# Kernel optimization log

Measured on AMD Instinct MI355X. Metric: run time of the kernel, lower is better.

The kernel has to match this reference:

```python
import jax, jax.numpy as jnp
import numpy as np
from jax import lax

LOG2PI = float(np.log(2.0 * np.pi))
N_K, N_T, N_C, N_D, N_SPK = 256, 128, 32, 10, 1000000

def _std_normal_logpdf(x):
    return -0.5 * (x * x + LOG2PI)

def _normal_logpdf(x, mu, log_sig):
    z = (x - mu) * jnp.exp(-log_sig)
    return -0.5 * (z * z + LOG2PI) - log_sig

def safe_log(x, minval=1e-10):
    return jnp.log(x + minval)

def setup_inputs() -> dict:
    key = jax.random.key(0)
    ks_ = jax.random.split(key, 8)
    s = jax.random.normal(ks_[0], (N_SPK, N_D), dtype=jnp.float32)
    y = jax.random.normal(ks_[1], (N_K, N_T), dtype=jnp.float32)
    ks = jax.random.randint(ks_[2], (N_SPK,), 0, N_K, dtype=jnp.int32)
    ts = jax.random.randint(ks_[3], (N_SPK,), 0, N_T, dtype=jnp.int32)
    means = jax.random.normal(ks_[4], (N_C, N_D), dtype=jnp.float32)
    A = jax.random.normal(ks_[5], (N_C, N_D, N_D), dtype=jnp.float32)
    covs = jnp.einsum('cij,ckj->cik', A, A) / N_D + jnp.eye(N_D, dtype=jnp.float32)
    b_mu = jax.random.normal(ks_[6], (N_C,), dtype=jnp.float32)
    b_log_sig = jax.random.normal(ks_[7], (N_C,), dtype=jnp.float32)
    beta_mu = jax.random.normal(jax.random.fold_in(key, 10), (N_C, N_T), dtype=jnp.float32)
    beta_log_sig = jax.random.normal(jax.random.fold_in(key, 11), (N_C, N_T), dtype=jnp.float32)
    return {"s": s, "y": y, "ks": ks, "ts": ts, "means": means, "covs": covs,
            "b_mu": b_mu, "b_log_sig": b_log_sig, "beta_mu": beta_mu, "beta_log_sig": beta_log_sig}

def _mvn_ll(s, means, covs):
    # ll[n, c] = MVN(means[c], covs[c]).log_prob(s[n]); loop over small n_c via lax.map
    L = jnp.linalg.cholesky(covs)                       # (c, d, d)
    logdet = 2.0 * jnp.sum(jnp.log(jnp.diagonal(L, axis1=1, axis2=2)), axis=1)  # (c,)
    d = s.shape[1]
    def comp(args):
        mu, Lc, ld = args
        diff = s - mu                                   # (n, d)
        z = jax.scipy.linalg.solve_triangular(Lc, diff.T, lower=True)  # (d, n)
        return -0.5 * (d * LOG2PI + ld + jnp.sum(z * z, axis=0))       # (n,)
    return lax.map(comp, (means, L, logdet)).T          # (n, c)

def reference(s, y, ks, ts, means, covs, b_mu, b_log_sig, beta_mu, beta_log_sig):
    # sampling=False path: use variational means
    b_sample, beta_sample = b_mu, beta_mu               # (c,), (c, t)
    # log_lambdas[k, c, t] = b[c] + beta[c, t] * y[k, t]
    log_lambdas = b_sample[None, :, None] + beta_sample[None, :, :] * y[:, None, :]
    log_pis = jax.nn.log_softmax(log_lambdas, axis=1)   # (k, c, t)
    ll = _mvn_ll(s, means, covs)                        # (n, c)
    logits = ll + log_pis[ks, :, ts]                    # per-spike gather -> (n, c)
    r = jax.nn.softmax(logits, axis=1)                  # responsibilities (n, c)
    log_prior = jnp.sum(_std_normal_logpdf(b_sample)) + jnp.sum(_std_normal_logpdf(beta_sample))
    log_q = jnp.sum(_normal_logpdf(b_sample, b_mu, b_log_sig)) + \
            jnp.sum(_normal_logpdf(beta_sample, beta_mu, beta_log_sig))
    elbo = log_prior - log_q
    elbo += jnp.sum(r * logits)
    elbo -= jnp.sum(r * safe_log(r))
    return elbo
```

## Files before the change

### kernel.cpp

```cpp
#include <hip/hip_runtime.h>
#include <hip/hip_bf16.h>
#include <math.h>

#define NK 256
#define NT 128
#define NC 32
#define ND 10
#define NSPK 1000000
#define LOG2PI 1.8378770664093453f
#define NCHUNK ((NSPK + 255) / 256)
#define GRID 1024

#define FSTR 36
#define LDS_DW (256 * FSTR)

typedef __attribute__((ext_vector_type(8))) short short8;
typedef __attribute__((ext_vector_type(4))) float floatx4;
typedef __attribute__((ext_vector_type(2))) float floatx2;
typedef __attribute__((ext_vector_type(4))) int intx4;

union FragCvt { intx4 i; short8 s; };


__device__ inline unsigned pack_bf16(float a, float b) {
  __hip_bfloat16 ha = __float2bfloat16(a), hb = __float2bfloat16(b);
  unsigned short ua, ub;
  __builtin_memcpy(&ua, &ha, 2);
  __builtin_memcpy(&ub, &hb, 2);
  return (unsigned)ua | ((unsigned)ub << 16);
}

__global__ __attribute__((amdgpu_waves_per_eu(1, 4)))
void prep_kernel(const float* __restrict__ y,
                 const float* __restrict__ means,
                 const float* __restrict__ covs,
                 const float* __restrict__ b_mu,
                 const float* __restrict__ b_ls,
                 const float* __restrict__ beta_mu,
                 const float* __restrict__ beta_ls,
                 int* __restrict__ wt,
                 float* __restrict__ cpack,
                 float* __restrict__ pisT,
                 double* __restrict__ acc,
                 unsigned int* __restrict__ counter) {
  int blk = blockIdx.x;
  int tid = threadIdx.x;

  if (blk == 0) {
    int c = tid;
    if (c >= NC) return;

    float M[ND][ND];
    #pragma unroll
    for (int i = 0; i < ND; ++i)
      #pragma unroll
      for (int j = 0; j < ND; ++j)
        M[i][j] = covs[c * ND * ND + i * ND + j];

    float logdet = 0.f;
    #pragma unroll
    for (int j = 0; j < ND; ++j) {
      float d = M[j][j];
      #pragma unroll
      for (int k = 0; k < ND; ++k) if (k < j) d -= M[j][k] * M[j][k];
      float sq = sqrtf(d);
      M[j][j] = sq;
      logdet += 2.f * __logf(sq);
      float inv = 1.f / sq;
      #pragma unroll
      for (int i = 0; i < ND; ++i) {
        if (i > j) {
          float s2 = M[i][j];
          #pragma unroll
          for (int k = 0; k < ND; ++k) if (k < j) s2 -= M[i][k] * M[j][k];
          M[i][j] = s2 * inv;
        }
      }
    }

    #pragma unroll
    for (int j = 0; j < ND; ++j) {
      M[j][j] = 1.f / M[j][j];
      #pragma unroll
      for (int i = 0; i < ND; ++i) {
        if (i > j) {
          float s2 = 0.f;
          #pragma unroll
          for (int k = 0; k < ND; ++k) if (k >= j && k < i) s2 += M[i][k] * M[k][j];
          M[i][j] = -s2 / M[i][i];
        }
      }
    }

    float pd[ND];
    #pragma unroll
    for (int i = 0; i < ND; ++i) {
      #pragma unroll
      for (int jj = 0; jj < ND; ++jj) {
        if (jj >= i) {
          float s2 = 0.f;
          #pragma unroll
          for (int k = 0; k < ND; ++k) if (k >= jj) s2 += M[k][i] * M[k][jj];
          if (jj > i) M[i][jj] = s2;
          else pd[i] = s2;
        }
      }
    }

    float mu[ND], q[ND];
    #pragma unroll
    for (int i = 0; i < ND; ++i) mu[i] = means[c * ND + i];
    float muPmu = 0.f;
    #pragma unroll
    for (int i = 0; i < ND; ++i) {
      float a2 = pd[i] * mu[i];
      #pragma unroll
      for (int j = 0; j < ND; ++j) {
        if (j < i) a2 += M[j][i] * mu[j];
        if (j > i) a2 += M[i][j] * mu[j];
      }
      q[i] = a2;
      muPmu += mu[i] * a2;
    }
    float cst = -0.5f * ((float)ND * LOG2PI + logdet + muPmu);

    float wv[64];
    int p = 0;
    #pragma unroll
    for (int i = 0; i < ND; ++i)
      #pragma unroll
      for (int j = 0; j < ND; ++j)
        if (j >= i && !(i == 9 && j == 9))
          wv[p++] = (i == j) ? -0.5f * pd[i] : -M[i][j];
    #pragma unroll
    for (int i = 0; i < ND; ++i) wv[54 + i] = q[i];

    #pragma unroll
    for (int j = 0; j < 32; ++j) {
      float a = wv[2 * j], b = wv[2 * j + 1];
      float ah = __bfloat162float(__float2bfloat16(a));
      float bh = __bfloat162float(__float2bfloat16(b));
      wt[c * 32 + j] = (int)pack_bf16(ah, bh);
      wt[(32 + c) * 32 + j] = (int)pack_bf16(a - ah, b - bh);
    }
    cpack[c] = cst;
    cpack[32 + c] = -0.5f * pd[9];

  } else if (blk == 1) {
    float local = 0.f;
    for (int i = tid; i < NC; i += 256)
      local += fmaf(-0.5f * b_mu[i], b_mu[i], b_ls[i]);
    for (int i = tid; i < NC * NT; i += 256)
      local += fmaf(-0.5f * beta_mu[i], beta_mu[i], beta_ls[i]);
    #pragma unroll
    for (int off = 32; off > 0; off >>= 1) local += __shfl_down(local, off);
    __shared__ float red[4];
    if ((tid & 63) == 0) red[tid >> 6] = local;
    __syncthreads();
    if (tid == 0) {
      acc[0] = (double)(red[0] + red[1] + red[2] + red[3]);
      counter[0] = 0u;
    }

  } else {
    int id = (blk - 2) * 256 + tid;
    int t = id & (NT - 1);
    float yv = y[id];
    float v[NC];
    float m = -1e30f;
    #pragma unroll
    for (int c = 0; c < NC; ++c) {
      v[c] = fmaf(beta_mu[c * NT + t], yv, b_mu[c]);
      m = fmaxf(m, v[c]);
    }
    float ssum = 0.f;
    #pragma unroll
    for (int c = 0; c < NC; ++c) ssum += __expf(v[c] - m);
    float lz = m + __logf(ssum);
    float* outp = pisT + (size_t)id * NC;
    #pragma unroll
    for (int c = 0; c < NC; ++c) outp[c] = v[c] - lz;
  }
}

__global__ __launch_bounds__(256) __attribute__((amdgpu_waves_per_eu(4, 4)))
void spike_kernel(const float* __restrict__ s,
                  const int* __restrict__ ks,
                  const int* __restrict__ ts,
                  const int* __restrict__ wt,
                  const float* __restrict__ cpack,
                  const float* __restrict__ pisT,
                  double* __restrict__ acc,
                  unsigned int* __restrict__ counter,
                  float* __restrict__ out) {
  __shared__ int lds[LDS_DW];
  __shared__ float red[4];

  int tid = threadIdx.x;
  int wv_ = tid >> 6, L = tid & 63;
  int r = L & 15, q = L >> 4;

  static constexpr int TI[64] = {
    0,0,0,0,0,0,0,0,0,0,
    1,1,1,1,1,1,1,1,1,
    2,2,2,2,2,2,2,2,
    3,3,3,3,3,3,3,
    4,4,4,4,4,4,
    5,5,5,5,5,
    6,6,6,6,
    7,7,7,
    8,8,
    0,1,2,3,4,5,6,7,8,9};
  static constexpr int TJ[64] = {
    0,1,2,3,4,5,6,7,8,9,
    1,2,3,4,5,6,7,8,9,
    2,3,4,5,6,7,8,9,
    3,4,5,6,7,8,9,
    4,5,6,7,8,9,
    5,6,7,8,9,
    6,7,8,9,
    7,8,9,
    8,9,
    -1,-1,-1,-1,-1,-1,-1,-1,-1,-1};

  FragCvt bf[2][2][2];
  #pragma unroll
  for (int h = 0; h < 2; ++h)
    #pragma unroll
    for (int nt = 0; nt < 2; ++nt)
      #pragma unroll
      for (int k2 = 0; k2 < 2; ++k2)
        bf[h][nt][k2].i =
            *(const intx4*)&wt[(h * 32 + nt * 16 + r) * 32 + k2 * 16 + q * 4];

  float lse_sum = 0.f;

  int ci = blockIdx.x;
  floatx4 sA, sB; floatx2 sC; int kk, tt;
  {
    int n = ci * 256 + tid;
    int nc = n < NSPK ? n : (NSPK - 1);
    const float* srow = s + (size_t)nc * ND;
    sA = __builtin_nontemporal_load((const floatx4*)srow);
    sB = __builtin_nontemporal_load((const floatx4*)(srow + 4));
    sC = __builtin_nontemporal_load((const floatx2*)(srow + 8));
    kk = __builtin_nontemporal_load(ks + nc);
    tt = __builtin_nontemporal_load(ts + nc);
  }

  for (; ci < NCHUNK; ci += GRID) {
    int n = ci * 256 + tid;
    float sv[10] = {sA.x, sA.y, sA.z, sA.w, sB.x, sB.y, sB.z, sB.w, sC.x, sC.y};
    float s9sq = sv[9] * sv[9];

    const float4* lpp = (const float4*)(pisT + (size_t)(kk * NT + tt) * NC);
    float4 lpv[8];
    #pragma unroll
    for (int i = 0; i < 8; ++i) lpv[i] = lpp[i];

    int cn = ci + GRID;
    if (cn < NCHUNK) {
      int n2 = cn * 256 + tid;
      int nc2 = n2 < NSPK ? n2 : (NSPK - 1);
      const float* srow2 = s + (size_t)nc2 * ND;
      sA = __builtin_nontemporal_load((const floatx4*)srow2);
      sB = __builtin_nontemporal_load((const floatx4*)(srow2 + 4));
      sC = __builtin_nontemporal_load((const floatx2*)(srow2 + 8));
      kk = __builtin_nontemporal_load(ks + nc2);
      tt = __builtin_nontemporal_load(ts + nc2);
    }

    {
      int rb = tid * FSTR;
      #pragma unroll
      for (int ch = 0; ch < 8; ++ch) {
        float t_[8];
        #pragma unroll
        for (int e = 0; e < 8; ++e) {
          int p = 8 * ch + e;
          t_[e] = (TJ[p] < 0) ? sv[TI[p]] : sv[TI[p]] * sv[TJ[p]];
        }
        intx4 v;
        v.x = (int)pack_bf16(t_[0], t_[1]);
        v.y = (int)pack_bf16(t_[2], t_[3]);
        v.z = (int)pack_bf16(t_[4], t_[5]);
        v.w = (int)pack_bf16(t_[6], t_[7]);
        *(intx4*)&lds[rb + ch * 4] = v;
      }
    }

    floatx4 accf[4][2];
    #pragma unroll
    for (int mt = 0; mt < 4; ++mt)
      #pragma unroll
      for (int nt = 0; nt < 2; ++nt)
        accf[mt][nt] = (floatx4){0.f, 0.f, 0.f, 0.f};

    #pragma unroll
    for (int mt = 0; mt < 4; ++mt) {
      #pragma unroll
      for (int k2 = 0; k2 < 2; ++k2) {
        FragCvt a;
        a.i = *(const intx4*)&lds[(wv_ * 64 + mt * 16 + r) * FSTR + k2 * 16 + q * 4];
        #pragma unroll
        for (int nt = 0; nt < 2; ++nt) {
          accf[mt][nt] = __builtin_amdgcn_mfma_f32_16x16x32_bf16(
              a.s, bf[0][nt][k2].s, accf[mt][nt], 0, 0, 0);
          accf[mt][nt] = __builtin_amdgcn_mfma_f32_16x16x32_bf16(
              a.s, bf[1][nt][k2].s, accf[mt][nt], 0, 0, 0);
        }
      }
    }

    #pragma unroll
    for (int mt = 0; mt < 4; ++mt)
      #pragma unroll
      for (int nt = 0; nt < 2; ++nt)
        #pragma unroll
        for (int rr = 0; rr < 4; ++rr) {
          int srow_ = wv_ * 64 + mt * 16 + q * 4 + rr;
          lds[srow_ * FSTR + nt * 16 + r] = __float_as_int(accf[mt][nt][rr]);
        }

    {
      float lp[32];
      #pragma unroll
      for (int i = 0; i < 8; ++i) {
        lp[4 * i + 0] = lpv[i].x; lp[4 * i + 1] = lpv[i].y;
        lp[4 * i + 2] = lpv[i].z; lp[4 * i + 3] = lpv[i].w;
      }
      int base = tid * FSTR;
      float lg[32];
      #pragma unroll
      for (int g = 0; g < 8; ++g) {
        intx4 lv = *(const intx4*)&lds[base + g * 4];
        lg[4 * g + 0] = __int_as_float(lv.x);
        lg[4 * g + 1] = __int_as_float(lv.y);
        lg[4 * g + 2] = __int_as_float(lv.z);
        lg[4 * g + 3] = __int_as_float(lv.w);
      }
      #pragma unroll
      for (int c = 0; c < 32; ++c)
        lg[c] += lp[c] + fmaf(cpack[32 + c], s9sq, cpack[c]);

      float m16[16];
      #pragma unroll
      for (int c = 0; c < 16; ++c) m16[c] = fmaxf(lg[c], lg[c + 16]);
      float m8[8];
      #pragma unroll
      for (int c = 0; c < 8; ++c) m8[c] = fmaxf(m16[c], m16[c + 8]);
      float m4[4];
      #pragma unroll
      for (int c = 0; c < 4; ++c) m4[c] = fmaxf(m8[c], m8[c + 4]);
      float m = fmaxf(fmaxf(m4[0], m4[1]), fmaxf(m4[2], m4[3]));

      float ss0 = 0.f, ss1 = 0.f, ss2 = 0.f, ss3 = 0.f;
      #pragma unroll
      for (int c = 0; c < 8; ++c) {
        ss0 += __expf(lg[4 * c + 0] - m);
        ss1 += __expf(lg[4 * c + 1] - m);
        ss2 += __expf(lg[4 * c + 2] - m);
        ss3 += __expf(lg[4 * c + 3] - m);
      }
      float ssum = (ss0 + ss1) + (ss2 + ss3);
      if (n < NSPK) lse_sum += m + __logf(ssum);
    }
  }

  #pragma unroll
  for (int off = 32; off > 0; off >>= 1) lse_sum += __shfl_down(lse_sum, off);
  if ((tid & 63) == 0) red[tid >> 6] = lse_sum;
  __syncthreads();
  if (tid == 0) {
    atomicAdd(acc, (double)(red[0] + red[1] + red[2] + red[3]));
    __threadfence();
    unsigned int old = atomicAdd(counter, 1u);
    if (old == GRID - 1) {
      __threadfence();
      double v = atomicAdd(acc, 0.0);
      out[0] = (float)v;
    }
  }
}

extern "C" void kernel_launch(void* const* d_in, const int* in_sizes, int n_in,
                              void* d_out, int out_size, void* d_ws, size_t ws_size,
                              hipStream_t stream) {
  const float* s       = (const float*)d_in[0];
  const float* y       = (const float*)d_in[1];
  const int*   ks      = (const int*)d_in[2];
  const int*   ts      = (const int*)d_in[3];
  const float* means   = (const float*)d_in[4];
  const float* covs    = (const float*)d_in[5];
  const float* b_mu    = (const float*)d_in[6];
  const float* b_ls    = (const float*)d_in[7];
  const float* beta_mu = (const float*)d_in[8];
  const float* beta_ls = (const float*)d_in[9];
  float* out = (float*)d_out;

  char* ws = (char*)d_ws;
  double* acc           = (double*)ws;
  unsigned int* counter = (unsigned int*)(ws + 8);
  float* cpack          = (float*)(ws + 64);
  int* wt               = (int*)(ws + 1024);
  float* pisT           = (float*)(ws + 16384);

  prep_kernel<<<2 + (NK * NT) / 256, 256, 0, stream>>>(
      y, means, covs, b_mu, b_ls, beta_mu, beta_ls, wt, cpack, pisT, acc, counter);
  spike_kernel<<<GRID, 256, 0, stream>>>(
      s, ks, ts, wt, cpack, pisT, acc, counter, out);
}
```

Before: 167.3 us.

## Factor log-softmax table into per-(k,t) normalizer plus per-t beta row

Instead of a 4 MB table of log_pis for every (k,t,c), the prep kernel stores only y and the log-normalizer per (k,t), plus beta transposed per t. The spike kernel rebuilds b+beta*y on the fly and subtracts the normalizer once per spike. This cuts the random 128-byte gather per spike down to an 8-byte gather plus a read of a small 16 KB beta table that stays in cache. It adds 32 extra FMAs per spike, and prep now stages beta_mu through shared memory.

```diff
diff --git a/kernel.cpp b/kernel.cpp
--- a/kernel.cpp
+++ b/kernel.cpp
@@ -40,7 +40,8 @@
                  const float* __restrict__ beta_ls,
                  int* __restrict__ wt,
                  float* __restrict__ cpack,
-                 float* __restrict__ pisT,
+                 float* __restrict__ betaT,
+                 float* __restrict__ yz,
                  double* __restrict__ acc,
                  unsigned int* __restrict__ counter) {
   int blk = blockIdx.x;
@@ -143,7 +144,7 @@
       wt[c * 32 + j] = (int)pack_bf16(ah, bh);
       wt[(32 + c) * 32 + j] = (int)pack_bf16(a - ah, b - bh);
     }
-    cpack[c] = cst;
+    cpack[c] = cst + b_mu[c];
     cpack[32 + c] = -0.5f * pd[9];
 
   } else if (blk == 1) {
@@ -163,6 +164,10 @@
     }
 
   } else {
+    __shared__ float bsh[NC * NT];
+    for (int i = tid; i < NC * NT; i += 256) bsh[i] = beta_mu[i];
+    __syncthreads();
+
     int id = (blk - 2) * 256 + tid;
     int t = id & (NT - 1);
     float yv = y[id];
@@ -170,16 +175,21 @@
     float m = -1e30f;
     #pragma unroll
     for (int c = 0; c < NC; ++c) {
-      v[c] = fmaf(beta_mu[c * NT + t], yv, b_mu[c]);
+      v[c] = fmaf(bsh[c * NT + t], yv, b_mu[c]);
       m = fmaxf(m, v[c]);
     }
     float ssum = 0.f;
     #pragma unroll
     for (int c = 0; c < NC; ++c) ssum += __expf(v[c] - m);
     float lz = m + __logf(ssum);
-    float* outp = pisT + (size_t)id * NC;
-    #pragma unroll
-    for (int c = 0; c < NC; ++c) outp[c] = v[c] - lz;
+    ((floatx2*)yz)[id] = (floatx2){yv, lz};
+
+    if (blk == 2) {
+      for (int i = tid; i < NC * NT; i += 256) {
+        int tt2 = i >> 5, cc2 = i & 31;
+        betaT[i] = bsh[cc2 * NT + tt2];
+      }
+    }
   }
 }
 
@@ -189,7 +199,8 @@
                   const int* __restrict__ ts,
                   const int* __restrict__ wt,
                   const float* __restrict__ cpack,
-                  const float* __restrict__ pisT,
+                  const float* __restrict__ betaT,
+                  const float* __restrict__ yz,
                   double* __restrict__ acc,
                   unsigned int* __restrict__ counter,
                   float* __restrict__ out) {
@@ -252,11 +263,9 @@
     int n = ci * 256 + tid;
     float sv[10] = {sA.x, sA.y, sA.z, sA.w, sB.x, sB.y, sB.z, sB.w, sC.x, sC.y};
     float s9sq = sv[9] * sv[9];
-
-    const float4* lpp = (const float4*)(pisT + (size_t)(kk * NT + tt) * NC);
-    float4 lpv[8];
-    #pragma unroll
-    for (int i = 0; i < 8; ++i) lpv[i] = lpp[i];
+    int myt = tt;
+
+    floatx2 yzv = ((const floatx2*)yz)[kk * NT + tt];
 
     int cn = ci + GRID;
     if (cn < NCHUNK) {
@@ -323,12 +332,6 @@
         }
 
     {
-      float lp[32];
-      #pragma unroll
-      for (int i = 0; i < 8; ++i) {
-        lp[4 * i + 0] = lpv[i].x; lp[4 * i + 1] = lpv[i].y;
-        lp[4 * i + 2] = lpv[i].z; lp[4 * i + 3] = lpv[i].w;
-      }
       int base = tid * FSTR;
       float lg[32];
       #pragma unroll
@@ -339,9 +342,15 @@
         lg[4 * g + 2] = __int_as_float(lv.z);
         lg[4 * g + 3] = __int_as_float(lv.w);
       }
-      #pragma unroll
-      for (int c = 0; c < 32; ++c)
-        lg[c] += lp[c] + fmaf(cpack[32 + c], s9sq, cpack[c]);
+      const float4* btp = (const float4*)(betaT + myt * NC);
+      #pragma unroll
+      for (int g = 0; g < 8; ++g) {
+        float4 b4 = btp[g];
+        lg[4 * g + 0] += fmaf(b4.x, yzv.x, fmaf(cpack[32 + 4*g+0], s9sq, cpack[4*g+0]));
+        lg[4 * g + 1] += fmaf(b4.y, yzv.x, fmaf(cpack[32 + 4*g+1], s9sq, cpack[4*g+1]));
+        lg[4 * g + 2] += fmaf(b4.z, yzv.x, fmaf(cpack[32 + 4*g+2], s9sq, cpack[4*g+2]));
+        lg[4 * g + 3] += fmaf(b4.w, yzv.x, fmaf(cpack[32 + 4*g+3], s9sq, cpack[4*g+3]));
+      }
 
       float m16[16];
       #pragma unroll
@@ -363,7 +372,7 @@
         ss3 += __expf(lg[4 * c + 3] - m);
       }
       float ssum = (ss0 + ss1) + (ss2 + ss3);
-      if (n < NSPK) lse_sum += m + __logf(ssum);
+      if (n < NSPK) lse_sum += m + __logf(ssum) - yzv.y;
     }
   }
 
@@ -403,10 +412,11 @@
   unsigned int* counter = (unsigned int*)(ws + 8);
   float* cpack          = (float*)(ws + 64);
   int* wt               = (int*)(ws + 1024);
-  float* pisT           = (float*)(ws + 16384);
+  float* betaT          = (float*)(ws + 12288);
+  float* yz             = (float*)(ws + 32768);
 
   prep_kernel<<<2 + (NK * NT) / 256, 256, 0, stream>>>(
-      y, means, covs, b_mu, b_ls, beta_mu, beta_ls, wt, cpack, pisT, acc, counter);
+      y, means, covs, b_mu, b_ls, beta_mu, beta_ls, wt, cpack, betaT, yz, acc, counter);
   spike_kernel<<<GRID, 256, 0, stream>>>(
-      s, ks, ts, wt, cpack, pisT, acc, counter, out);
+      s, ks, ts, wt, cpack, betaT, yz, acc, counter, out);
 }
```

After: 160.0 us. 4.4% less time.
